# Kernel optimization log

Measured on AMD Instinct MI355X. Metric: run time of the kernel, lower is better.

Reference implementation:

```python
import jax, jax.numpy as jnp
import numpy as np

N_NODES = 50000
N_EDGES = 800000
D = 64            # NODE_FEATURE_DIM == EDGE_FEATURE_DIM
H = 128           # EDGE_FEATURE_HIDDEN
EDGE_STEPS = 4
NODE_STEPS = 2


def _mlp2(h, W1, b1, W2, b2):
    # two-layer MLP with ReLU between (bn=False, end_with_relu=False)
    return jnp.maximum(h @ W1 + b1, 0.0) @ W2 + b2


def setup_inputs() -> dict:
    key = jax.random.key(0)
    ks = iter(jax.random.split(key, 40))

    def w(shape):
        fan_in = shape[0]
        return jax.random.normal(next(ks), shape, dtype=jnp.float32) / np.sqrt(fan_in)

    inp = {
        "x": jax.random.normal(next(ks), (N_NODES, 128), dtype=jnp.float32),
        "edge_attr": jax.random.normal(next(ks), (N_EDGES, 19), dtype=jnp.float32),
        "edge_index": jax.random.randint(next(ks), (2, N_EDGES), 0, N_NODES),
        "node_types": jax.random.randint(next(ks), (N_NODES,), 0, 17),
        # node embedding MLP: 128 -> 64 -> 64
        "ne_W1": w((128, D)), "ne_b1": jnp.zeros((D,)), "ne_W2": w((D, D)), "ne_b2": jnp.zeros((D,)),
        # edge embedding MLP: 19 -> 64 -> 64
        "ee_W1": w((19, D)), "ee_b1": jnp.zeros((D,)), "ee_W2": w((D, D)), "ee_b2": jnp.zeros((D,)),
        # MPN edge MLP: [x_src(2D), x_dst(2D), e(2D)] = 384 -> 128 -> 64
        "mp_eW1": w((6 * D, H)), "mp_eb1": jnp.zeros((H,)), "mp_eW2": w((H, D)), "mp_eb2": jnp.zeros((D,)),
        # MPN node-update MLP: 64 -> 64
        "mp_nW": w((D, D)), "mp_nb": jnp.zeros((D,)),
        # edge classification head: 64 -> 32 -> 1
        "ec_W1": w((D, 32)), "ec_b1": jnp.zeros((32,)), "ec_W2": w((32, 1)), "ec_b2": jnp.zeros((1,)),
        # node classification head: 64 -> 32 -> 1
        "nc_W1": w((D, 32)), "nc_b1": jnp.zeros((32,)), "nc_W2": w((32, 1)), "nc_b2": jnp.zeros((1,)),
        # type classification head: 64 -> 32 -> 17
        "cl_W1": w((D, 32)), "cl_b1": jnp.zeros((32,)), "cl_W2": w((32, 17)), "cl_b2": jnp.zeros((17,)),
    }
    return inp


def reference(x, edge_attr, edge_index, node_types,
              ne_W1, ne_b1, ne_W2, ne_b2,
              ee_W1, ee_b1, ee_W2, ee_b2,
              mp_eW1, mp_eb1, mp_eW2, mp_eb2,
              mp_nW, mp_nb,
              ec_W1, ec_b1, ec_W2, ec_b2,
              nc_W1, nc_b1, nc_W2, nc_b2,
              cl_W1, cl_b1, cl_W2, cl_b2):
    src, dst = edge_index[0], edge_index[1]

    nf0 = _mlp2(x, ne_W1, ne_b1, ne_W2, ne_b2)          # [N, D] initial node emb
    ef0 = _mlp2(edge_attr, ee_W1, ee_b1, ee_W2, ee_b2)  # [E, D] initial edge emb
    nf, ef = nf0, ef0

    def mpn_step(nf, ef):
        # skip connections: concat initial features each iteration
        nf_c = jnp.concatenate([nf0, nf], axis=1)   # [N, 2D]
        ef_c = jnp.concatenate([ef0, ef], axis=1)   # [E, 2D]
        msg_in = jnp.concatenate([nf_c[src], nf_c[dst], ef_c], axis=1)  # [E, 6D]
        e_new = _mlp2(msg_in, mp_eW1, mp_eb1, mp_eW2, mp_eb2)           # [E, D]
        agg = jax.ops.segment_sum(e_new, dst, num_segments=N_NODES)    # [N, D]
        n_new = jnp.maximum(agg @ mp_nW + mp_nb, 0.0)                   # [N, D]
        return n_new, e_new

    for _ in range(EDGE_STEPS):
        nf, ef = mpn_step(nf, ef)
    pred_edge = _mlp2(ef, ec_W1, ec_b1, ec_W2, ec_b2).squeeze(-1)  # [E]

    for _ in range(NODE_STEPS):
        nf, ef = mpn_step(nf, ef)
    pred_node = _mlp2(nf, nc_W1, nc_b1, nc_W2, nc_b2).squeeze(-1)  # [N]
    pred_class = _mlp2(nf, cl_W1, cl_b1, cl_W2, cl_b2)             # [N, 17]

    return (pred_edge, pred_node, pred_class)
```

## Files before the change

kernel.cpp:

```cpp
#include <hip/hip_runtime.h>

#define NN 50000
#define EE 800000

typedef unsigned short u16;
typedef __attribute__((ext_vector_type(8))) short bf16x8;
typedef __attribute__((ext_vector_type(4))) float f32x4;

#define MFMA16(a, b, c) __builtin_amdgcn_mfma_f32_16x16x32_bf16(a, b, c, 0, 0, 0)

__device__ __forceinline__ float bf2f(u16 v) {
    union { unsigned u; float f; } x; x.u = ((unsigned)v) << 16; return x.f;
}
__device__ __forceinline__ u16 f2bf(float f) {
    union { float f; unsigned u; } x; x.f = f;
    unsigned r = x.u + 0x7FFFu + ((x.u >> 16) & 1u);
    return (u16)(r >> 16);
}
__device__ __forceinline__ void gl_lds16(const u16* g, u16* l) {
    __builtin_amdgcn_global_load_lds((const __attribute__((address_space(1))) void*)g,
                                     (__attribute__((address_space(3))) void*)l, 16, 0, 0);
}

__global__ void pack_frag(const float* __restrict__ W, u16* __restrict__ dst, int K, int N) {
    int i = blockIdx.x * 256 + threadIdx.x;
    int nfc = N / 16, kkc = (K + 31) / 32;
    int total = kkc * nfc * 512;
    if (i >= total) return;
    int t = i & 7, lane = (i >> 3) & 63;
    int rest = i >> 9;
    int nf = rest % nfc, kk = rest / nfc;
    int k = kk * 32 + (lane >> 4) * 8 + t, n = nf * 16 + (lane & 15);
    dst[i] = (k < K) ? f2bf(W[k * N + n]) : (u16)0;
}

__global__ __launch_bounds__(256) void embed_mfma_node(
    const float* __restrict__ x, const u16* __restrict__ pW1, const float* __restrict__ b1,
    const u16* __restrict__ pW2, const float* __restrict__ b2, u16* __restrict__ out)
{
    __shared__ alignas(16) u16 A[64 * 136];
    __shared__ alignas(16) u16 Hs[64 * 72];
    int tid = threadIdx.x;
    size_t row0 = (size_t)blockIdx.x * 64;
    #pragma unroll
    for (int it = 0; it < 8; ++it) {
        int u = it * 256 + tid;
        int row = u >> 5, seg = u & 31;
        float4 v = (row0 + row < NN) ? *(const float4*)(x + (row0 + row) * 128 + seg * 4)
                                     : make_float4(0.f, 0.f, 0.f, 0.f);
        ushort4 o; o.x = f2bf(v.x); o.y = f2bf(v.y); o.z = f2bf(v.z); o.w = f2bf(v.w);
        *(ushort4*)(A + row * 136 + seg * 4) = o;
    }
    __syncthreads();
    int wave = tid >> 6, lane = tid & 63, l15 = lane & 15, l4 = lane >> 4;
    int col = wave * 16 + l15;
    f32x4 acc[4] = {};
    #pragma unroll
    for (int kk = 0; kk < 4; ++kk) {
        bf16x8 b = *(const bf16x8*)(pW1 + (size_t)((kk * 4 + wave) * 64 + lane) * 8);
        #pragma unroll
        for (int mi = 0; mi < 4; ++mi) {
            bf16x8 a = *(const bf16x8*)(A + (mi * 16 + l15) * 136 + kk * 32 + l4 * 8);
            acc[mi] = MFMA16(a, b, acc[mi]);
        }
    }
    float bias = b1[col];
    #pragma unroll
    for (int mi = 0; mi < 4; ++mi)
        #pragma unroll
        for (int r = 0; r < 4; ++r) {
            float v = acc[mi][r] + bias;
            Hs[(mi * 16 + l4 * 4 + r) * 72 + col] = f2bf(v > 0.f ? v : 0.f);
        }
    __syncthreads();
    f32x4 acc2[4] = {};
    #pragma unroll
    for (int kk = 0; kk < 2; ++kk) {
        bf16x8 b = *(const bf16x8*)(pW2 + (size_t)((kk * 4 + wave) * 64 + lane) * 8);
        #pragma unroll
        for (int mi = 0; mi < 4; ++mi) {
            bf16x8 a = *(const bf16x8*)(Hs + (mi * 16 + l15) * 72 + kk * 32 + l4 * 8);
            acc2[mi] = MFMA16(a, b, acc2[mi]);
        }
    }
    float bias2 = b2[col];
    __syncthreads();
    #pragma unroll
    for (int mi = 0; mi < 4; ++mi)
        #pragma unroll
        for (int r = 0; r < 4; ++r)
            Hs[(mi * 16 + l4 * 4 + r) * 72 + col] = f2bf(acc2[mi][r] + bias2);
    __syncthreads();
    #pragma unroll
    for (int it = 0; it < 4; ++it) {
        int u = it * 256 + tid;
        int row = u >> 4, c4 = (u & 15) * 4;
        if (row0 + row < NN) {
            ushort4 o = *(const ushort4*)(Hs + row * 72 + c4);
            *(ushort4*)(out + (row0 + row) * 64 + c4) = o;
        }
    }
}

__global__ __launch_bounds__(256) void embed_mfma_edge(
    const float* __restrict__ ea, const int* __restrict__ eids,
    const u16* __restrict__ pW1, const float* __restrict__ b1,
    const u16* __restrict__ pW2, const float* __restrict__ b2, u16* __restrict__ out)
{
    __shared__ alignas(16) u16 A[64 * 40];
    __shared__ alignas(16) u16 Hs[64 * 72];
    __shared__ int eid_s[64];
    int tid = threadIdx.x;
    size_t row0 = (size_t)blockIdx.x * 64;
    if (tid < 64) eid_s[tid] = eids[row0 + tid];
    __syncthreads();
    #pragma unroll
    for (int it = 0; it < 8; ++it) {
        int u = it * 256 + tid;
        int row = u >> 5, k = u & 31;
        float v = (k < 19) ? ea[(size_t)eid_s[row] * 19 + k] : 0.f;
        A[row * 40 + k] = f2bf(v);
    }
    __syncthreads();
    int wave = tid >> 6, lane = tid & 63, l15 = lane & 15, l4 = lane >> 4;
    int col = wave * 16 + l15;
    f32x4 acc[4] = {};
    {
        bf16x8 b = *(const bf16x8*)(pW1 + (size_t)(wave * 64 + lane) * 8);
        #pragma unroll
        for (int mi = 0; mi < 4; ++mi) {
            bf16x8 a = *(const bf16x8*)(A + (mi * 16 + l15) * 40 + l4 * 8);
            acc[mi] = MFMA16(a, b, acc[mi]);
        }
    }
    float bias = b1[col];
    #pragma unroll
    for (int mi = 0; mi < 4; ++mi)
        #pragma unroll
        for (int r = 0; r < 4; ++r) {
            float v = acc[mi][r] + bias;
            Hs[(mi * 16 + l4 * 4 + r) * 72 + col] = f2bf(v > 0.f ? v : 0.f);
        }
    __syncthreads();
    f32x4 acc2[4] = {};
    #pragma unroll
    for (int kk = 0; kk < 2; ++kk) {
        bf16x8 b = *(const bf16x8*)(pW2 + (size_t)((kk * 4 + wave) * 64 + lane) * 8);
        #pragma unroll
        for (int mi = 0; mi < 4; ++mi) {
            bf16x8 a = *(const bf16x8*)(Hs + (mi * 16 + l15) * 72 + kk * 32 + l4 * 8);
            acc2[mi] = MFMA16(a, b, acc2[mi]);
        }
    }
    float bias2 = b2[col];
    __syncthreads();
    #pragma unroll
    for (int mi = 0; mi < 4; ++mi)
        #pragma unroll
        for (int r = 0; r < 4; ++r)
            Hs[(mi * 16 + l4 * 4 + r) * 72 + col] = f2bf(acc2[mi][r] + bias2);
    __syncthreads();
    #pragma unroll
    for (int it = 0; it < 4; ++it) {
        int u = it * 256 + tid;
        int row = u >> 4, c4 = (u & 15) * 4;
        ushort4 o = *(const ushort4*)(Hs + row * 72 + c4);
        *(ushort4*)(out + (row0 + row) * 64 + c4) = o;
    }
}

__global__ void zero_cnt(int* __restrict__ cnt) {
    int i = blockIdx.x * 256 + threadIdx.x;
    if (i < NN) cnt[i] = 0;
}
__global__ void count_deg(const int* __restrict__ eidx, int* __restrict__ cnt) {
    int e = blockIdx.x * 256 + threadIdx.x;
    if (e < EE) atomicAdd(&cnt[eidx[EE + e]], 1);
}
__global__ void scan_k(const int* __restrict__ cnt, int* __restrict__ starts) {
    __shared__ int part[1024];
    int t = threadIdx.x;
    const int chunk = (NN + 1023) / 1024;
    int lo = t * chunk, hi = lo + chunk; if (hi > NN) hi = NN;
    if (lo > NN) lo = NN;
    int s = 0;
    for (int i = lo; i < hi; ++i) s += cnt[i];
    part[t] = s;
    __syncthreads();
    for (int off = 1; off < 1024; off <<= 1) {
        int v = part[t];
        int add = (t >= off) ? part[t - off] : 0;
        __syncthreads();
        part[t] = v + add;
        __syncthreads();
    }
    int run = (t == 0) ? 0 : part[t - 1];
    for (int i = lo; i < hi; ++i) { starts[i] = run; run += cnt[i]; }
    if (t == 1023) starts[NN] = EE;
}
__global__ void init_cur(const int* __restrict__ starts, int* __restrict__ cur) {
    int i = blockIdx.x * 256 + threadIdx.x;
    if (i < NN) cur[i] = starts[i];
}
__global__ void scatter_e(const int* __restrict__ eidx, int* __restrict__ cur,
                          int* __restrict__ eids) {
    int e = blockIdx.x * 256 + threadIdx.x;
    if (e < EE) {
        int pos = atomicAdd(&cur[eidx[EE + e]], 1);
        eids[pos] = e;
    }
}
__global__ void build_perm(const int* __restrict__ eidx, const int* __restrict__ eids,
                           int* __restrict__ psrc, int* __restrict__ pdst) {
    int j = blockIdx.x * 256 + threadIdx.x;
    if (j < EE) {
        int e = eids[j];
        psrc[j] = eidx[e];
        pdst[j] = eidx[EE + e];
    }
}

__global__ __launch_bounds__(256, 3) void edge_mlp(
    const int* __restrict__ psrc, const int* __restrict__ pdst,
    const u16* __restrict__ nf0, const u16* __restrict__ nfc,
    const u16* __restrict__ ef0, const u16* __restrict__ efc,
    const u16* __restrict__ pW1, const u16* __restrict__ pW2,
    const float* __restrict__ eb1, const float* __restrict__ eb2,
    u16* __restrict__ efn)
{
    __shared__ alignas(16) u16 Chunk[6][64 * 64];
    const int tid = threadIdx.x;
    const int tile0 = blockIdx.x * 64;
    const int wave = tid >> 6, lane = tid & 63;
    const int l15 = lane & 15, l4 = lane >> 4;

    const int r0 = wave * 16 + (lane >> 3);
    const int r1 = r0 + 8;
    const int u_ = lane & 7;
    const int su0 = u_ ^ (r0 & 7);
    const int su1 = u_ ^ (r1 & 7);
    const int is0 = psrc[tile0 + r0] * 64;
    const int is1 = psrc[tile0 + r1] * 64;
    const int id0 = pdst[tile0 + r0] * 64;
    const int id1 = pdst[tile0 + r1] * 64;

    bf16x8 bw[24];
    #pragma unroll
    for (int kk = 0; kk < 12; ++kk) {
        bw[kk * 2 + 0] = *(const bf16x8*)(pW1 + (size_t)((kk * 8 + wave * 2 + 0) * 64 + lane) * 8);
        bw[kk * 2 + 1] = *(const bf16x8*)(pW1 + (size_t)((kk * 8 + wave * 2 + 1) * 64 + lane) * 8);
    }
    #pragma unroll
    for (int i = 0; i < 24; ++i) asm volatile("" : "+v"(bw[i]));
    __builtin_amdgcn_sched_barrier(0);

    #pragma unroll
    for (int c = 0; c < 6; ++c) {
        const u16 *b0, *b1;
        if (c == 0)      { b0 = nf0 + is0; b1 = nf0 + is1; }
        else if (c == 1) { b0 = nfc + is0; b1 = nfc + is1; }
        else if (c == 2) { b0 = nf0 + id0; b1 = nf0 + id1; }
        else if (c == 3) { b0 = nfc + id0; b1 = nfc + id1; }
        else if (c == 4) { b0 = ef0 + (size_t)(tile0 + r0) * 64; b1 = ef0 + (size_t)(tile0 + r1) * 64; }
        else             { b0 = efc + (size_t)(tile0 + r0) * 64; b1 = efc + (size_t)(tile0 + r1) * 64; }
        u16* l0 = (u16*)Chunk + c * 4096 + wave * 1024;
        gl_lds16(b0 + su0 * 8, l0);
        gl_lds16(b1 + su1 * 8, l0 + 512);
    }
    __builtin_amdgcn_sched_barrier(0);

    f32x4 acc[4][2] = {};
    #pragma unroll
    for (int c = 0; c < 6; ++c) {
        if (c == 0)      asm volatile("s_waitcnt vmcnt(10)" ::: "memory");
        else if (c == 1) asm volatile("s_waitcnt vmcnt(8)" ::: "memory");
        else if (c == 2) asm volatile("s_waitcnt vmcnt(6)" ::: "memory");
        else if (c == 3) asm volatile("s_waitcnt vmcnt(4)" ::: "memory");
        else if (c == 4) asm volatile("s_waitcnt vmcnt(2)" ::: "memory");
        else             asm volatile("s_waitcnt vmcnt(0)" ::: "memory");
        __builtin_amdgcn_s_barrier();
        __builtin_amdgcn_sched_barrier(0);
        const char* Cb = (const char*)Chunk + c * 8192;
        #pragma unroll
        for (int kkl = 0; kkl < 2; ++kkl) {
            const int kk = c * 2 + kkl;
            #pragma unroll
            for (int mi = 0; mi < 4; ++mi) {
                int row = mi * 16 + l15;
                bf16x8 a = *(const bf16x8*)(Cb + row * 128 + ((kkl * 64 + l4 * 16) ^ ((row & 7) << 4)));
                acc[mi][0] = MFMA16(a, bw[kk * 2 + 0], acc[mi][0]);
                acc[mi][1] = MFMA16(a, bw[kk * 2 + 1], acc[mi][1]);
            }
        }
    }

    char* HidB = (char*)Chunk;
    #pragma unroll
    for (int nj = 0; nj < 2; ++nj) {
        int col = wave * 32 + nj * 16 + l15;
        float bias = eb1[col];
        #pragma unroll
        for (int mi = 0; mi < 4; ++mi) {
            #pragma unroll
            for (int r = 0; r < 4; ++r) {
                int row = mi * 16 + l4 * 4 + r;
                float v = acc[mi][nj][r] + bias;
                v = v > 0.f ? v : 0.f;
                *(u16*)(HidB + row * 256 + ((col * 2) ^ ((row & 7) << 4))) = f2bf(v);
            }
        }
    }
    __syncthreads();

    f32x4 acc2[4] = {};
    const int m0 = wave * 16;
    #pragma unroll
    for (int kk = 0; kk < 4; ++kk) {
        int row = m0 + l15;
        bf16x8 a = *(const bf16x8*)(HidB + row * 256 + ((kk * 64 + l4 * 16) ^ ((row & 7) << 4)));
        #pragma unroll
        for (int nf = 0; nf < 4; ++nf) {
            bf16x8 b = *(const bf16x8*)(pW2 + (size_t)((kk * 4 + nf) * 64 + lane) * 8);
            acc2[nf] = MFMA16(a, b, acc2[nf]);
        }
    }

    float* EnF = (float*)((char*)Chunk + 16384);
    #pragma unroll
    for (int nf = 0; nf < 4; ++nf) {
        int col = nf * 16 + l15;
        float bias = eb2[col];
        #pragma unroll
        for (int r = 0; r < 4; ++r) {
            int row = m0 + l4 * 4 + r;
            EnF[row * 64 + col] = acc2[nf][r] + bias;
        }
    }
    __syncthreads();
    #pragma unroll
    for (int rep = 0; rep < 4; ++rep) {
        int u = rep * 256 + tid;
        int el = u >> 4, d0 = (u & 15) * 4;
        const float* s = EnF + el * 64 + d0;
        ushort4 o;
        o.x = f2bf(s[0]); o.y = f2bf(s[1]); o.z = f2bf(s[2]); o.w = f2bf(s[3]);
        *(ushort4*)(efn + (size_t)(tile0 + el) * 64 + d0) = o;
    }
}

__global__ __launch_bounds__(256) void node_update(
    const u16* __restrict__ enewp,
    const int* __restrict__ starts,
    const float* __restrict__ Wn, const float* __restrict__ bn,
    u16* __restrict__ nfn)
{
    __shared__ float Wns[64 * 64];
    int tid = threadIdx.x;
    for (int i = tid; i < 4096; i += 256) Wns[i] = Wn[i];
    __syncthreads();
    const int l = tid & 63;
    const int q = l & 15;
    const int base = l & 48;
    const int n = blockIdx.x * 16 + (tid >> 4);
    if (n >= NN) return;
    const int s0 = starts[n], s1 = starts[n + 1];
    const int cnt = s1 - s0;
    const u16* p = enewp + (size_t)s0 * 64 + q * 4;
    float a0 = 0.f, a1 = 0.f, a2 = 0.f, a3 = 0.f;
    int i = 0;
    for (; i + 4 <= cnt; i += 4) {
        ushort4 v0 = *(const ushort4*)(p + (i + 0) * 64);
        ushort4 v1 = *(const ushort4*)(p + (i + 1) * 64);
        ushort4 v2 = *(const ushort4*)(p + (i + 2) * 64);
        ushort4 v3 = *(const ushort4*)(p + (i + 3) * 64);
        a0 += bf2f(v0.x) + bf2f(v1.x) + bf2f(v2.x) + bf2f(v3.x);
        a1 += bf2f(v0.y) + bf2f(v1.y) + bf2f(v2.y) + bf2f(v3.y);
        a2 += bf2f(v0.z) + bf2f(v1.z) + bf2f(v2.z) + bf2f(v3.z);
        a3 += bf2f(v0.w) + bf2f(v1.w) + bf2f(v2.w) + bf2f(v3.w);
    }
    for (; i < cnt; ++i) {
        ushort4 v0 = *(const ushort4*)(p + i * 64);
        a0 += bf2f(v0.x); a1 += bf2f(v0.y); a2 += bf2f(v0.z); a3 += bf2f(v0.w);
    }
    const float4 bb = *(const float4*)(bn + q * 4);
    float o0 = bb.x, o1 = bb.y, o2 = bb.z, o3 = bb.w;
    #pragma unroll
    for (int hq = 0; hq < 16; ++hq) {
        int src = base | hq;
        float b0 = __shfl(a0, src), b1 = __shfl(a1, src);
        float b2 = __shfl(a2, src), b3 = __shfl(a3, src);
        const float4 w0 = *(const float4*)(Wns + (hq * 4 + 0) * 64 + q * 4);
        const float4 w1 = *(const float4*)(Wns + (hq * 4 + 1) * 64 + q * 4);
        const float4 w2 = *(const float4*)(Wns + (hq * 4 + 2) * 64 + q * 4);
        const float4 w3 = *(const float4*)(Wns + (hq * 4 + 3) * 64 + q * 4);
        o0 += b0 * w0.x + b1 * w1.x + b2 * w2.x + b3 * w3.x;
        o1 += b0 * w0.y + b1 * w1.y + b2 * w2.y + b3 * w3.y;
        o2 += b0 * w0.z + b1 * w1.z + b2 * w2.z + b3 * w3.z;
        o3 += b0 * w0.w + b1 * w1.w + b2 * w2.w + b3 * w3.w;
    }
    ushort4 o;
    o.x = f2bf(o0 > 0.f ? o0 : 0.f);
    o.y = f2bf(o1 > 0.f ? o1 : 0.f);
    o.z = f2bf(o2 > 0.f ? o2 : 0.f);
    o.w = f2bf(o3 > 0.f ? o3 : 0.f);
    *(ushort4*)(nfn + (size_t)n * 64 + q * 4) = o;
}

__global__ __launch_bounds__(256) void edge_head(
    const u16* __restrict__ ef, const int* __restrict__ eids,
    const u16* __restrict__ pW1, const float* __restrict__ b1,
    const float* __restrict__ W2, const float* __restrict__ b2, float* __restrict__ out)
{
    __shared__ alignas(16) u16 A[64 * 72];
    int tid = threadIdx.x;
    int tile0 = blockIdx.x * 64;
    #pragma unroll
    for (int it = 0; it < 2; ++it) {
        int u = it * 256 + tid;
        int row = u >> 3, sub = u & 7;
        uint4 v = *(const uint4*)(ef + (size_t)(tile0 + row) * 64 + sub * 8);
        *(uint4*)(A + row * 72 + sub * 8) = v;
    }
    __syncthreads();
    int wave = tid >> 6, lane = tid & 63, l15 = lane & 15, l4 = lane >> 4;
    int m0 = wave * 16;
    f32x4 acc[2] = {};
    #pragma unroll
    for (int kk = 0; kk < 2; ++kk) {
        bf16x8 a = *(const bf16x8*)(A + (m0 + l15) * 72 + kk * 32 + l4 * 8);
        #pragma unroll
        for (int nf = 0; nf < 2; ++nf) {
            bf16x8 b = *(const bf16x8*)(pW1 + (size_t)((kk * 2 + nf) * 64 + lane) * 8);
            acc[nf] = MFMA16(a, b, acc[nf]);
        }
    }
    float bias2 = b2[0];
    #pragma unroll
    for (int r = 0; r < 4; ++r) {
        float p = 0.f;
        #pragma unroll
        for (int nf = 0; nf < 2; ++nf) {
            int col = nf * 16 + l15;
            float h = acc[nf][r] + b1[col];
            p += (h > 0.f ? h : 0.f) * W2[col];
        }
        p += __shfl_xor(p, 1); p += __shfl_xor(p, 2);
        p += __shfl_xor(p, 4); p += __shfl_xor(p, 8);
        if (l15 == 0) out[eids[tile0 + m0 + l4 * 4 + r]] = p + bias2;
    }
}

__global__ void node_head(const u16* __restrict__ nf,
                          const float* __restrict__ ncW1, const float* __restrict__ ncb1,
                          const float* __restrict__ ncW2, const float* __restrict__ ncb2,
                          const float* __restrict__ clW1, const float* __restrict__ clb1,
                          const float* __restrict__ clW2, const float* __restrict__ clb2,
                          float* __restrict__ outN, float* __restrict__ outC) {
    __shared__ float sNW1[2048], sCW1[2048], sCW2[32 * 17];
    __shared__ float sNb1[32], sCb1[32], sNW2[32], sCb2[17];
    int tid = threadIdx.x;
    for (int i = tid; i < 2048; i += 256) { sNW1[i] = ncW1[i]; sCW1[i] = clW1[i]; }
    for (int i = tid; i < 544; i += 256) sCW2[i] = clW2[i];
    if (tid < 32) { sNb1[tid] = ncb1[tid]; sCb1[tid] = clb1[tid]; sNW2[tid] = ncW2[tid]; }
    if (tid < 17) sCb2[tid] = clb2[tid];
    __syncthreads();
    int n = blockIdx.x * 256 + tid;
    if (n >= NN) return;
    const u16* r = nf + (size_t)n * 64;
    float v[64];
    for (int k4 = 0; k4 < 16; ++k4) {
        ushort4 q = *(const ushort4*)(r + k4 * 4);
        v[k4 * 4 + 0] = bf2f(q.x); v[k4 * 4 + 1] = bf2f(q.y);
        v[k4 * 4 + 2] = bf2f(q.z); v[k4 * 4 + 3] = bf2f(q.w);
    }
    float h[32];
    #pragma unroll
    for (int j = 0; j < 32; ++j) h[j] = sNb1[j];
    for (int k = 0; k < 64; ++k) {
        float vk = v[k];
        #pragma unroll
        for (int j = 0; j < 32; ++j) h[j] += vk * sNW1[k * 32 + j];
    }
    float o = ncb2[0];
    #pragma unroll
    for (int j = 0; j < 32; ++j) o += (h[j] > 0.f ? h[j] : 0.f) * sNW2[j];
    outN[n] = o;
    #pragma unroll
    for (int j = 0; j < 32; ++j) h[j] = sCb1[j];
    for (int k = 0; k < 64; ++k) {
        float vk = v[k];
        #pragma unroll
        for (int j = 0; j < 32; ++j) h[j] += vk * sCW1[k * 32 + j];
    }
    float oc[17];
    #pragma unroll
    for (int c = 0; c < 17; ++c) oc[c] = sCb2[c];
    #pragma unroll
    for (int j = 0; j < 32; ++j) {
        float hr = h[j] > 0.f ? h[j] : 0.f;
        #pragma unroll
        for (int c = 0; c < 17; ++c) oc[c] += hr * sCW2[j * 17 + c];
    }
    #pragma unroll
    for (int c = 0; c < 17; ++c) outC[(size_t)n * 17 + c] = oc[c];
}

extern "C" void kernel_launch(void* const* d_in, const int* in_sizes, int n_in,
                              void* d_out, int out_size, void* d_ws, size_t ws_size,
                              hipStream_t stream) {
    const float* x     = (const float*)d_in[0];
    const float* ea    = (const float*)d_in[1];
    const int*   eidx  = (const int*)d_in[2];
    const float* neW1  = (const float*)d_in[4];
    const float* neb1  = (const float*)d_in[5];
    const float* neW2  = (const float*)d_in[6];
    const float* neb2  = (const float*)d_in[7];
    const float* eeW1  = (const float*)d_in[8];
    const float* eeb1  = (const float*)d_in[9];
    const float* eeW2  = (const float*)d_in[10];
    const float* eeb2  = (const float*)d_in[11];
    const float* mpW1  = (const float*)d_in[12];
    const float* mpb1  = (const float*)d_in[13];
    const float* mpW2  = (const float*)d_in[14];
    const float* mpb2  = (const float*)d_in[15];
    const float* mpnW  = (const float*)d_in[16];
    const float* mpnb  = (const float*)d_in[17];
    const float* ecW1  = (const float*)d_in[18];
    const float* ecb1  = (const float*)d_in[19];
    const float* ecW2  = (const float*)d_in[20];
    const float* ecb2  = (const float*)d_in[21];
    const float* ncW1  = (const float*)d_in[22];
    const float* ncb1  = (const float*)d_in[23];
    const float* ncW2  = (const float*)d_in[24];
    const float* ncb2  = (const float*)d_in[25];
    const float* clW1  = (const float*)d_in[26];
    const float* clb1  = (const float*)d_in[27];
    const float* clW2  = (const float*)d_in[28];
    const float* clb2  = (const float*)d_in[29];

    char* w = (char*)d_ws;
    size_t used = 0;
    auto alloc = [&](size_t b) {
        char* p = w + used; used += (b + 255) & ~(size_t)255; return p;
    };
    u16* nf0  = (u16*)alloc((size_t)NN * 64 * 2);
    u16* nfW  = (u16*)alloc((size_t)NN * 64 * 2);
    u16* ef0  = (u16*)alloc((size_t)EE * 64 * 2);
    u16* efW  = (u16*)alloc((size_t)EE * 64 * 2);
    u16* pmW1 = (u16*)alloc(49152 * 2);
    u16* pmW2 = (u16*)alloc(8192 * 2);
    u16* pnW1 = (u16*)alloc(8192 * 2);
    u16* pnW2 = (u16*)alloc(4096 * 2);
    u16* peW1 = (u16*)alloc(2048 * 2);
    u16* peW2 = (u16*)alloc(4096 * 2);
    u16* pcW1 = (u16*)alloc(2048 * 2);
    int* cnt    = (int*)alloc((size_t)NN * 4);
    int* starts = (int*)alloc((size_t)(NN + 1) * 4);
    int* eids   = (int*)alloc((size_t)EE * 4);
    int* psrc   = (int*)alloc((size_t)EE * 4);
    int* pdst   = (int*)alloc((size_t)EE * 4);
    if (used > ws_size) return;

    pack_frag<<<192, 256, 0, stream>>>(mpW1, pmW1, 384, 128);
    pack_frag<<<32, 256, 0, stream>>>(mpW2, pmW2, 128, 64);
    pack_frag<<<32, 256, 0, stream>>>(neW1, pnW1, 128, 64);
    pack_frag<<<16, 256, 0, stream>>>(neW2, pnW2, 64, 64);
    pack_frag<<<8, 256, 0, stream>>>(eeW1, peW1, 19, 64);
    pack_frag<<<16, 256, 0, stream>>>(eeW2, peW2, 64, 64);
    pack_frag<<<8, 256, 0, stream>>>(ecW1, pcW1, 64, 32);

    zero_cnt<<<(NN + 255) / 256, 256, 0, stream>>>(cnt);
    count_deg<<<EE / 256, 256, 0, stream>>>(eidx, cnt);
    scan_k<<<1, 1024, 0, stream>>>(cnt, starts);
    init_cur<<<(NN + 255) / 256, 256, 0, stream>>>(starts, cnt);
    scatter_e<<<EE / 256, 256, 0, stream>>>(eidx, cnt, eids);
    build_perm<<<EE / 256, 256, 0, stream>>>(eidx, eids, psrc, pdst);

    embed_mfma_node<<<(NN + 63) / 64, 256, 0, stream>>>(x, pnW1, neb1, pnW2, neb2, nf0);
    embed_mfma_edge<<<EE / 64, 256, 0, stream>>>(ea, eids, peW1, eeb1, peW2, eeb2, ef0);

    float* outE = (float*)d_out;
    float* outN = outE + EE;
    float* outC = outN + NN;

    const u16* nfc = nf0;
    const u16* efc = ef0;
    for (int s = 0; s < 6; ++s) {
        edge_mlp<<<EE / 64, 256, 0, stream>>>(psrc, pdst, nf0, nfc, ef0, efc,
                                              pmW1, pmW2, mpb1, mpb2, efW);
        node_update<<<(NN + 15) / 16, 256, 0, stream>>>(efW, starts, mpnW, mpnb, nfW);
        if (s == 3)
            edge_head<<<EE / 64, 256, 0, stream>>>(efW, eids, pcW1, ecb1, ecW2, ecb2, outE);
        efc = efW;
        nfc = nfW;
    }
    node_head<<<(NN + 255) / 256, 256, 0, stream>>>(nfc, ncW1, ncb1, ncW2, ncb2,
                                                    clW1, clb1, clW2, clb2, outN, outC);
    (void)in_sizes; (void)n_in; (void)out_size;
}
```

Baseline: 1.238 ms.

## Restructure edge MLP so each wave owns 16 rows with direct global A loads

Each wave now handles its own 16 edges across all 128 hidden columns. It loads A fragments straight from global memory instead of staging a 64-row tile in LDS through global_load_lds with block barriers, and it streams W1 fragments from global instead of keeping them resident in registers. LDS shrinks to a small per-wave scratch, block-level syncs are dropped, and occupancy is raised to 4 blocks per SM. In exchange, W1 is reloaded from cache for every MFMA group, and the gathered rows are read with less coalesced 16-byte per-lane loads that are no longer prefetched ahead of compute.

```diff
diff --git a/kernel.cpp b/kernel.cpp
--- a/kernel.cpp
+++ b/kernel.cpp
@@ -16,10 +16,6 @@
     union { float f; unsigned u; } x; x.f = f;
     unsigned r = x.u + 0x7FFFu + ((x.u >> 16) & 1u);
     return (u16)(r >> 16);
-}
-__device__ __forceinline__ void gl_lds16(const u16* g, u16* l) {
-    __builtin_amdgcn_global_load_lds((const __attribute__((address_space(1))) void*)g,
-                                     (__attribute__((address_space(3))) void*)l, 16, 0, 0);
 }
 
 __global__ void pack_frag(const float* __restrict__ W, u16* __restrict__ dst, int K, int N) {
@@ -220,7 +216,7 @@
     }
 }
 
-__global__ __launch_bounds__(256, 3) void edge_mlp(
+__global__ __launch_bounds__(256, 4) void edge_mlp(
     const int* __restrict__ psrc, const int* __restrict__ pdst,
     const u16* __restrict__ nf0, const u16* __restrict__ nfc,
     const u16* __restrict__ ef0, const u16* __restrict__ efc,
@@ -228,123 +224,85 @@
     const float* __restrict__ eb1, const float* __restrict__ eb2,
     u16* __restrict__ efn)
 {
-    __shared__ alignas(16) u16 Chunk[6][64 * 64];
+    __shared__ alignas(16) u16 X[4][16 * 132];
     const int tid = threadIdx.x;
     const int tile0 = blockIdx.x * 64;
     const int wave = tid >> 6, lane = tid & 63;
     const int l15 = lane & 15, l4 = lane >> 4;
-
-    const int r0 = wave * 16 + (lane >> 3);
-    const int r1 = r0 + 8;
-    const int u_ = lane & 7;
-    const int su0 = u_ ^ (r0 & 7);
-    const int su1 = u_ ^ (r1 & 7);
-    const int is0 = psrc[tile0 + r0] * 64;
-    const int is1 = psrc[tile0 + r1] * 64;
-    const int id0 = pdst[tile0 + r0] * 64;
-    const int id1 = pdst[tile0 + r1] * 64;
-
-    bf16x8 bw[24];
-    #pragma unroll
-    for (int kk = 0; kk < 12; ++kk) {
-        bw[kk * 2 + 0] = *(const bf16x8*)(pW1 + (size_t)((kk * 8 + wave * 2 + 0) * 64 + lane) * 8);
-        bw[kk * 2 + 1] = *(const bf16x8*)(pW1 + (size_t)((kk * 8 + wave * 2 + 1) * 64 + lane) * 8);
-    }
-    #pragma unroll
-    for (int i = 0; i < 24; ++i) asm volatile("" : "+v"(bw[i]));
-    __builtin_amdgcn_sched_barrier(0);
-
+    const int m0 = wave * 16;
+    const int rI = tile0 + m0 + l15;
+    const int koff = l4 * 8;
+
+    const int rs = psrc[rI] * 64;
+    const int rd = pdst[rI] * 64;
+    const int re = rI * 64;
+
+    f32x4 acc[8] = {};
     #pragma unroll
     for (int c = 0; c < 6; ++c) {
-        const u16 *b0, *b1;
-        if (c == 0)      { b0 = nf0 + is0; b1 = nf0 + is1; }
-        else if (c == 1) { b0 = nfc + is0; b1 = nfc + is1; }
-        else if (c == 2) { b0 = nf0 + id0; b1 = nf0 + id1; }
-        else if (c == 3) { b0 = nfc + id0; b1 = nfc + id1; }
-        else if (c == 4) { b0 = ef0 + (size_t)(tile0 + r0) * 64; b1 = ef0 + (size_t)(tile0 + r1) * 64; }
-        else             { b0 = efc + (size_t)(tile0 + r0) * 64; b1 = efc + (size_t)(tile0 + r1) * 64; }
-        u16* l0 = (u16*)Chunk + c * 4096 + wave * 1024;
-        gl_lds16(b0 + su0 * 8, l0);
-        gl_lds16(b1 + su1 * 8, l0 + 512);
-    }
-    __builtin_amdgcn_sched_barrier(0);
-
-    f32x4 acc[4][2] = {};
-    #pragma unroll
-    for (int c = 0; c < 6; ++c) {
-        if (c == 0)      asm volatile("s_waitcnt vmcnt(10)" ::: "memory");
-        else if (c == 1) asm volatile("s_waitcnt vmcnt(8)" ::: "memory");
-        else if (c == 2) asm volatile("s_waitcnt vmcnt(6)" ::: "memory");
-        else if (c == 3) asm volatile("s_waitcnt vmcnt(4)" ::: "memory");
-        else if (c == 4) asm volatile("s_waitcnt vmcnt(2)" ::: "memory");
-        else             asm volatile("s_waitcnt vmcnt(0)" ::: "memory");
-        __builtin_amdgcn_s_barrier();
-        __builtin_amdgcn_sched_barrier(0);
-        const char* Cb = (const char*)Chunk + c * 8192;
+        const u16* rp;
+        if (c == 0)      rp = nf0 + rs;
+        else if (c == 1) rp = nfc + rs;
+        else if (c == 2) rp = nf0 + rd;
+        else if (c == 3) rp = nfc + rd;
+        else if (c == 4) rp = ef0 + re;
+        else             rp = efc + re;
         #pragma unroll
         for (int kkl = 0; kkl < 2; ++kkl) {
             const int kk = c * 2 + kkl;
+            bf16x8 a = *(const bf16x8*)(rp + kkl * 32 + koff);
             #pragma unroll
-            for (int mi = 0; mi < 4; ++mi) {
-                int row = mi * 16 + l15;
-                bf16x8 a = *(const bf16x8*)(Cb + row * 128 + ((kkl * 64 + l4 * 16) ^ ((row & 7) << 4)));
-                acc[mi][0] = MFMA16(a, bw[kk * 2 + 0], acc[mi][0]);
-                acc[mi][1] = MFMA16(a, bw[kk * 2 + 1], acc[mi][1]);
+            for (int n = 0; n < 8; ++n) {
+                bf16x8 b = *(const bf16x8*)(pW1 + (size_t)((kk * 8 + n) * 64 + lane) * 8);
+                acc[n] = MFMA16(a, b, acc[n]);
             }
         }
     }
 
-    char* HidB = (char*)Chunk;
-    #pragma unroll
-    for (int nj = 0; nj < 2; ++nj) {
-        int col = wave * 32 + nj * 16 + l15;
-        float bias = eb1[col];
-        #pragma unroll
-        for (int mi = 0; mi < 4; ++mi) {
-            #pragma unroll
-            for (int r = 0; r < 4; ++r) {
-                int row = mi * 16 + l4 * 4 + r;
-                float v = acc[mi][nj][r] + bias;
-                v = v > 0.f ? v : 0.f;
-                *(u16*)(HidB + row * 256 + ((col * 2) ^ ((row & 7) << 4))) = f2bf(v);
-            }
-        }
-    }
-    __syncthreads();
+    u16* Xw = X[wave];
+    #pragma unroll
+    for (int n = 0; n < 8; ++n) {
+        float bias = eb1[n * 16 + l15];
+        #pragma unroll
+        for (int r = 0; r < 4; ++r) {
+            float v = acc[n][r] + bias;
+            Xw[(l4 * 4 + r) * 132 + n * 16 + l15] = f2bf(v > 0.f ? v : 0.f);
+        }
+    }
+    asm volatile("s_waitcnt lgkmcnt(0)" ::: "memory");
 
     f32x4 acc2[4] = {};
-    const int m0 = wave * 16;
     #pragma unroll
     for (int kk = 0; kk < 4; ++kk) {
-        int row = m0 + l15;
-        bf16x8 a = *(const bf16x8*)(HidB + row * 256 + ((kk * 64 + l4 * 16) ^ ((row & 7) << 4)));
+        bf16x8 a = *(const bf16x8*)(Xw + l15 * 132 + kk * 32 + koff);
         #pragma unroll
         for (int nf = 0; nf < 4; ++nf) {
             bf16x8 b = *(const bf16x8*)(pW2 + (size_t)((kk * 4 + nf) * 64 + lane) * 8);
             acc2[nf] = MFMA16(a, b, acc2[nf]);
         }
     }
-
-    float* EnF = (float*)((char*)Chunk + 16384);
+    asm volatile("s_waitcnt lgkmcnt(0)" ::: "memory");
+
+    float* Xf = (float*)Xw;
     #pragma unroll
     for (int nf = 0; nf < 4; ++nf) {
-        int col = nf * 16 + l15;
-        float bias = eb2[col];
-        #pragma unroll
-        for (int r = 0; r < 4; ++r) {
-            int row = m0 + l4 * 4 + r;
-            EnF[row * 64 + col] = acc2[nf][r] + bias;
-        }
-    }
-    __syncthreads();
-    #pragma unroll
-    for (int rep = 0; rep < 4; ++rep) {
-        int u = rep * 256 + tid;
-        int el = u >> 4, d0 = (u & 15) * 4;
-        const float* s = EnF + el * 64 + d0;
-        ushort4 o;
-        o.x = f2bf(s[0]); o.y = f2bf(s[1]); o.z = f2bf(s[2]); o.w = f2bf(s[3]);
-        *(ushort4*)(efn + (size_t)(tile0 + el) * 64 + d0) = o;
+        float bias = eb2[nf * 16 + l15];
+        #pragma unroll
+        for (int r = 0; r < 4; ++r)
+            Xf[(l4 * 4 + r) * 66 + nf * 16 + l15] = acc2[nf][r] + bias;
+    }
+    asm volatile("s_waitcnt lgkmcnt(0)" ::: "memory");
+    {
+        int row = lane >> 2, c0 = (lane & 3) * 16;
+        const float* s = Xf + row * 66 + c0;
+        u16* dst = efn + (size_t)(tile0 + m0 + row) * 64 + c0;
+        #pragma unroll
+        for (int j = 0; j < 4; ++j) {
+            ushort4 o;
+            o.x = f2bf(s[j * 4 + 0]); o.y = f2bf(s[j * 4 + 1]);
+            o.z = f2bf(s[j * 4 + 2]); o.w = f2bf(s[j * 4 + 3]);
+            *(ushort4*)(dst + j * 4) = o;
+        }
     }
 }
 
```

Result: slower. 1.847 ms (+49.1%).

## Shrink edge_mlp LDS to 4 chunks with buffer reuse and fuse edge head

Applied to the files above, without the earlier changes.

Cuts the edge MLP's staging LDS from six 8KB chunks to four. The two edge-feature chunks are loaded into buffers freed after the first GEMM chunks, which allows launch bounds of 4 blocks per CU instead of 3. The edge classification head is folded into edge_mlp on step 3, reusing the fp32 output tile in LDS and removing a separate kernel launch plus its re-read of edge features. Risks: the added barriers serialise part of the gather pipeline, and the tighter occupancy bound may force register spilling given the 24 preloaded weight fragments.

```diff
diff --git a/kernel.cpp b/kernel.cpp
--- a/kernel.cpp
+++ b/kernel.cpp
@@ -220,15 +220,18 @@
     }
 }
 
-__global__ __launch_bounds__(256, 3) void edge_mlp(
+__global__ __launch_bounds__(256, 4) void edge_mlp(
     const int* __restrict__ psrc, const int* __restrict__ pdst,
     const u16* __restrict__ nf0, const u16* __restrict__ nfc,
     const u16* __restrict__ ef0, const u16* __restrict__ efc,
     const u16* __restrict__ pW1, const u16* __restrict__ pW2,
     const float* __restrict__ eb1, const float* __restrict__ eb2,
-    u16* __restrict__ efn)
+    u16* __restrict__ efn,
+    const int* __restrict__ eids, const u16* __restrict__ pcW1,
+    const float* __restrict__ hb1, const float* __restrict__ hW2,
+    const float* __restrict__ hb2, float* __restrict__ outE, int doHead)
 {
-    __shared__ alignas(16) u16 Chunk[6][64 * 64];
+    __shared__ alignas(16) u16 Chunk[4][64 * 64];
     const int tid = threadIdx.x;
     const int tile0 = blockIdx.x * 64;
     const int wave = tid >> 6, lane = tid & 63;
@@ -255,14 +258,12 @@
     __builtin_amdgcn_sched_barrier(0);
 
     #pragma unroll
-    for (int c = 0; c < 6; ++c) {
+    for (int c = 0; c < 4; ++c) {
         const u16 *b0, *b1;
         if (c == 0)      { b0 = nf0 + is0; b1 = nf0 + is1; }
         else if (c == 1) { b0 = nfc + is0; b1 = nfc + is1; }
         else if (c == 2) { b0 = nf0 + id0; b1 = nf0 + id1; }
-        else if (c == 3) { b0 = nfc + id0; b1 = nfc + id1; }
-        else if (c == 4) { b0 = ef0 + (size_t)(tile0 + r0) * 64; b1 = ef0 + (size_t)(tile0 + r1) * 64; }
-        else             { b0 = efc + (size_t)(tile0 + r0) * 64; b1 = efc + (size_t)(tile0 + r1) * 64; }
+        else             { b0 = nfc + id0; b1 = nfc + id1; }
         u16* l0 = (u16*)Chunk + c * 4096 + wave * 1024;
         gl_lds16(b0 + su0 * 8, l0);
         gl_lds16(b1 + su1 * 8, l0 + 512);
@@ -270,31 +271,62 @@
     __builtin_amdgcn_sched_barrier(0);
 
     f32x4 acc[4][2] = {};
-    #pragma unroll
-    for (int c = 0; c < 6; ++c) {
-        if (c == 0)      asm volatile("s_waitcnt vmcnt(10)" ::: "memory");
-        else if (c == 1) asm volatile("s_waitcnt vmcnt(8)" ::: "memory");
-        else if (c == 2) asm volatile("s_waitcnt vmcnt(6)" ::: "memory");
-        else if (c == 3) asm volatile("s_waitcnt vmcnt(4)" ::: "memory");
-        else if (c == 4) asm volatile("s_waitcnt vmcnt(2)" ::: "memory");
-        else             asm volatile("s_waitcnt vmcnt(0)" ::: "memory");
-        __builtin_amdgcn_s_barrier();
-        __builtin_amdgcn_sched_barrier(0);
-        const char* Cb = (const char*)Chunk + c * 8192;
+    auto gemm_chunk = [&](int buf, int kk0) {
+        const char* Cb = (const char*)Chunk + buf * 8192;
         #pragma unroll
         for (int kkl = 0; kkl < 2; ++kkl) {
-            const int kk = c * 2 + kkl;
             #pragma unroll
             for (int mi = 0; mi < 4; ++mi) {
                 int row = mi * 16 + l15;
                 bf16x8 a = *(const bf16x8*)(Cb + row * 128 + ((kkl * 64 + l4 * 16) ^ ((row & 7) << 4)));
-                acc[mi][0] = MFMA16(a, bw[kk * 2 + 0], acc[mi][0]);
-                acc[mi][1] = MFMA16(a, bw[kk * 2 + 1], acc[mi][1]);
+                acc[mi][0] = MFMA16(a, bw[(kk0 + kkl) * 2 + 0], acc[mi][0]);
+                acc[mi][1] = MFMA16(a, bw[(kk0 + kkl) * 2 + 1], acc[mi][1]);
             }
         }
-    }
-
-    char* HidB = (char*)Chunk;
+    };
+
+    asm volatile("s_waitcnt vmcnt(6)" ::: "memory");
+    __builtin_amdgcn_s_barrier();
+    __builtin_amdgcn_sched_barrier(0);
+    gemm_chunk(0, 0);
+    __builtin_amdgcn_s_barrier();
+    __builtin_amdgcn_sched_barrier(0);
+    {
+        u16* l0 = (u16*)Chunk + wave * 1024;
+        gl_lds16(ef0 + (size_t)(tile0 + r0) * 64 + su0 * 8, l0);
+        gl_lds16(ef0 + (size_t)(tile0 + r1) * 64 + su1 * 8, l0 + 512);
+    }
+    __builtin_amdgcn_sched_barrier(0);
+    asm volatile("s_waitcnt vmcnt(6)" ::: "memory");
+    __builtin_amdgcn_s_barrier();
+    __builtin_amdgcn_sched_barrier(0);
+    gemm_chunk(1, 2);
+    __builtin_amdgcn_s_barrier();
+    __builtin_amdgcn_sched_barrier(0);
+    {
+        u16* l0 = (u16*)Chunk + 4096 + wave * 1024;
+        gl_lds16(efc + (size_t)(tile0 + r0) * 64 + su0 * 8, l0);
+        gl_lds16(efc + (size_t)(tile0 + r1) * 64 + su1 * 8, l0 + 512);
+    }
+    __builtin_amdgcn_sched_barrier(0);
+    asm volatile("s_waitcnt vmcnt(6)" ::: "memory");
+    __builtin_amdgcn_s_barrier();
+    __builtin_amdgcn_sched_barrier(0);
+    gemm_chunk(2, 4);
+    asm volatile("s_waitcnt vmcnt(4)" ::: "memory");
+    __builtin_amdgcn_s_barrier();
+    __builtin_amdgcn_sched_barrier(0);
+    gemm_chunk(3, 6);
+    asm volatile("s_waitcnt vmcnt(2)" ::: "memory");
+    __builtin_amdgcn_s_barrier();
+    __builtin_amdgcn_sched_barrier(0);
+    gemm_chunk(0, 8);
+    asm volatile("s_waitcnt vmcnt(0)" ::: "memory");
+    __builtin_amdgcn_s_barrier();
+    __builtin_amdgcn_sched_barrier(0);
+    gemm_chunk(1, 10);
+
+    char* HidB = (char*)Chunk + 16384;
     #pragma unroll
     for (int nj = 0; nj < 2; ++nj) {
         int col = wave * 32 + nj * 16 + l15;
@@ -325,7 +357,7 @@
         }
     }
 
-    float* EnF = (float*)((char*)Chunk + 16384);
+    float* EnF = (float*)Chunk;
     #pragma unroll
     for (int nf = 0; nf < 4; ++nf) {
         int col = nf * 16 + l15;
@@ -345,6 +377,36 @@
         ushort4 o;
         o.x = f2bf(s[0]); o.y = f2bf(s[1]); o.z = f2bf(s[2]); o.w = f2bf(s[3]);
         *(ushort4*)(efn + (size_t)(tile0 + el) * 64 + d0) = o;
+    }
+
+    if (doHead) {
+        f32x4 hacc[2] = {};
+        #pragma unroll
+        for (int kk = 0; kk < 2; ++kk) {
+            const float* s = EnF + (m0 + l15) * 64 + kk * 32 + l4 * 8;
+            bf16x8 a;
+            #pragma unroll
+            for (int j = 0; j < 8; ++j) a[j] = (short)f2bf(s[j]);
+            #pragma unroll
+            for (int nf = 0; nf < 2; ++nf) {
+                bf16x8 b = *(const bf16x8*)(pcW1 + (size_t)((kk * 2 + nf) * 64 + lane) * 8);
+                hacc[nf] = MFMA16(a, b, hacc[nf]);
+            }
+        }
+        float bias2 = hb2[0];
+        #pragma unroll
+        for (int r = 0; r < 4; ++r) {
+            float p = 0.f;
+            #pragma unroll
+            for (int nf = 0; nf < 2; ++nf) {
+                int col = nf * 16 + l15;
+                float h = hacc[nf][r] + hb1[col];
+                p += (h > 0.f ? h : 0.f) * hW2[col];
+            }
+            p += __shfl_xor(p, 1); p += __shfl_xor(p, 2);
+            p += __shfl_xor(p, 4); p += __shfl_xor(p, 8);
+            if (l15 == 0) outE[eids[tile0 + m0 + l4 * 4 + r]] = p + bias2;
+        }
     }
 }
 
@@ -404,50 +466,6 @@
     o.z = f2bf(o2 > 0.f ? o2 : 0.f);
     o.w = f2bf(o3 > 0.f ? o3 : 0.f);
     *(ushort4*)(nfn + (size_t)n * 64 + q * 4) = o;
-}
-
-__global__ __launch_bounds__(256) void edge_head(
-    const u16* __restrict__ ef, const int* __restrict__ eids,
-    const u16* __restrict__ pW1, const float* __restrict__ b1,
-    const float* __restrict__ W2, const float* __restrict__ b2, float* __restrict__ out)
-{
-    __shared__ alignas(16) u16 A[64 * 72];
-    int tid = threadIdx.x;
-    int tile0 = blockIdx.x * 64;
-    #pragma unroll
-    for (int it = 0; it < 2; ++it) {
-        int u = it * 256 + tid;
-        int row = u >> 3, sub = u & 7;
-        uint4 v = *(const uint4*)(ef + (size_t)(tile0 + row) * 64 + sub * 8);
-        *(uint4*)(A + row * 72 + sub * 8) = v;
-    }
-    __syncthreads();
-    int wave = tid >> 6, lane = tid & 63, l15 = lane & 15, l4 = lane >> 4;
-    int m0 = wave * 16;
-    f32x4 acc[2] = {};
-    #pragma unroll
-    for (int kk = 0; kk < 2; ++kk) {
-        bf16x8 a = *(const bf16x8*)(A + (m0 + l15) * 72 + kk * 32 + l4 * 8);
-        #pragma unroll
-        for (int nf = 0; nf < 2; ++nf) {
-            bf16x8 b = *(const bf16x8*)(pW1 + (size_t)((kk * 2 + nf) * 64 + lane) * 8);
-            acc[nf] = MFMA16(a, b, acc[nf]);
-        }
-    }
-    float bias2 = b2[0];
-    #pragma unroll
-    for (int r = 0; r < 4; ++r) {
-        float p = 0.f;
-        #pragma unroll
-        for (int nf = 0; nf < 2; ++nf) {
-            int col = nf * 16 + l15;
-            float h = acc[nf][r] + b1[col];
-            p += (h > 0.f ? h : 0.f) * W2[col];
-        }
-        p += __shfl_xor(p, 1); p += __shfl_xor(p, 2);
-        p += __shfl_xor(p, 4); p += __shfl_xor(p, 8);
-        if (l15 == 0) out[eids[tile0 + m0 + l4 * 4 + r]] = p + bias2;
-    }
 }
 
 __global__ void node_head(const u16* __restrict__ nf,
@@ -587,10 +605,10 @@
     const u16* efc = ef0;
     for (int s = 0; s < 6; ++s) {
         edge_mlp<<<EE / 64, 256, 0, stream>>>(psrc, pdst, nf0, nfc, ef0, efc,
-                                              pmW1, pmW2, mpb1, mpb2, efW);
+                                              pmW1, pmW2, mpb1, mpb2, efW,
+                                              eids, pcW1, ecb1, ecW2, ecb2, outE,
+                                              (s == 3) ? 1 : 0);
         node_update<<<(NN + 15) / 16, 256, 0, stream>>>(efW, starts, mpnW, mpnb, nfW);
-        if (s == 3)
-            edge_head<<<EE / 64, 256, 0, stream>>>(efW, eids, pcW1, ecb1, ecW2, ecb2, outE);
         efc = efW;
         nfc = nfW;
     }
```

Result: slower. 1.397 ms (+12.8%).
